# Optimization experiments

Hardware: AMD Instinct MI355X
Metric: run time of the kernel (lower is better)

The kernel has to match this reference:

```python
import jax, jax.numpy as jnp
import numpy as np

B, S, F, H = 16, 2048, 1024, 16
D = F // H
EPS = 1e-5


def setup_inputs() -> dict:
    key = jax.random.key(0)
    ks = jax.random.split(key, 10)
    scale = 1.0 / np.sqrt(F)
    return {
        "x": jax.random.normal(ks[0], (B, S, F), jnp.float32),
        "Wq": jax.random.normal(ks[1], (F, F), jnp.float32) * scale,
        "bq": jnp.zeros((F,), jnp.float32),
        "Wk": jax.random.normal(ks[2], (F, F), jnp.float32) * scale,
        "bk": jnp.zeros((F,), jnp.float32),
        "Wv": jax.random.normal(ks[3], (F, F), jnp.float32) * scale,
        "bv": jnp.zeros((F,), jnp.float32),
        "Wo": jax.random.normal(ks[4], (F, F), jnp.float32) * scale,
        "bo": jnp.zeros((F,), jnp.float32),
        "gamma": jnp.ones((F,), jnp.float32),
        "beta": jnp.zeros((F,), jnp.float32),
    }


def reference(x, Wq, bq, Wk, bk, Wv, bv, Wo, bo, gamma, beta):
    # x: (B, S, F). Dropout is identity in eval mode.
    b, s, f = x.shape
    q = (x @ Wq + bq).reshape(b, s, H, D)
    k = (x @ Wk + bk).reshape(b, s, H, D)
    v = (x @ Wv + bv).reshape(b, s, H, D)
    # Faithful to source: the einsum (applied to permuted tensors) contracts
    # across HEADS at each sequence position -> scores (B, S, H, H).
    energy = jnp.einsum('bshd,bsgd->bshg', q, k) / (D ** 0.5)
    attn = jax.nn.softmax(energy, axis=-1)  # softmax over key-head axis
    out = jnp.einsum('bshg,bsgd->bshd', attn, v).reshape(b, s, f)
    out = out @ Wo + bo
    # LayerNorm over last dim (eps=1e-5, affine)
    mu = jnp.mean(out, axis=-1, keepdims=True)
    var = jnp.mean((out - mu) ** 2, axis=-1, keepdims=True)
    return (out - mu) * jax.lax.rsqrt(var + EPS) * gamma + beta
```

## Files before the change

### kernel.cpp

```cpp
#include <hip/hip_runtime.h>
#include <hip/hip_bf16.h>
#include <stdint.h>

#define MM   32768
#define FFD  1024
#define NQKV 3072

typedef __bf16 bf16x8 __attribute__((ext_vector_type(8)));
typedef float  f32x4  __attribute__((ext_vector_type(4)));

__device__ __forceinline__ unsigned short f2bf_bits(float f){
  __hip_bfloat16 h = __float2bfloat16(f);
  unsigned short u;
  __builtin_memcpy(&u, &h, 2);
  return u;
}

__device__ __forceinline__ void gld16(const void* g, void* l){
  const unsigned int* gu = (const unsigned int*)g;
  unsigned int* lu = (unsigned int*)l;
  __builtin_amdgcn_global_load_lds(
      (const __attribute__((address_space(1))) unsigned int*)gu,
      (__attribute__((address_space(3))) unsigned int*)lu,
      16, 0, 0);
}

__global__ __launch_bounds__(256) void k_convert_bf16(const float* __restrict__ in,
                                                      unsigned short* __restrict__ out,
                                                      int n4){
  int i = blockIdx.x * 256 + threadIdx.x;
  if (i >= n4) return;
  float4 v = ((const float4*)in)[i];
  ushort4 r;
  r.x = f2bf_bits(v.x); r.y = f2bf_bits(v.y);
  r.z = f2bf_bits(v.z); r.w = f2bf_bits(v.w);
  ((ushort4*)out)[i] = r;
}

__global__ __launch_bounds__(256) void k_transpose_bf16(const float* __restrict__ in,
                                                        unsigned short* __restrict__ out,
                                                        int rows, int cols){
  __shared__ float tile[32][33];
  int bc = blockIdx.x * 32, br = blockIdx.y * 32;
  int tx = threadIdx.x, ty = threadIdx.y;
  #pragma unroll
  for (int j = 0; j < 32; j += 8)
    tile[ty + j][tx] = in[(size_t)(br + ty + j) * cols + bc + tx];
  __syncthreads();
  #pragma unroll
  for (int j = 0; j < 32; j += 8)
    out[(size_t)(bc + ty + j) * rows + br + tx] = f2bf_bits(tile[tx][ty + j]);
}

template <bool BF16OUT>
__global__ __launch_bounds__(256) void k_gemm_bt(
    const unsigned short* __restrict__ A,
    const unsigned short* __restrict__ Bt,
    const float* __restrict__ b0, const float* __restrict__ b1, const float* __restrict__ b2,
    void* __restrict__ Cout, int M, int N, int K)
{
  __shared__ unsigned short As[128 * 64];
  __shared__ unsigned short Bs[128 * 64];

  const int tid  = threadIdx.x;
  const int lane = tid & 63;
  const int wave = tid >> 6;
  const int wr = wave >> 1, wc = wave & 1;
  const int quad = lane >> 4, lrow = lane & 15;

  const long rowBase = (long)blockIdx.y * 128;
  const long colBase = (long)blockIdx.x * 128;

  f32x4 acc[4][4];
  #pragma unroll
  for (int i = 0; i < 4; i++)
    #pragma unroll
    for (int j = 0; j < 4; j++)
      acc[i][j] = (f32x4){0.f, 0.f, 0.f, 0.f};

  const unsigned short* ga = A  + (rowBase + (tid >> 2)) * (long)K + (tid & 3) * 8;
  const unsigned short* gb = Bt + (colBase + (tid >> 2)) * (long)K + (tid & 3) * 8;
  unsigned short* la = As + tid * 8;
  unsigned short* lb = Bs + tid * 8;
  const long rstep = 64L * K;

  const int nk = K >> 6;
  for (int kt = 0; kt < nk; kt++){
    __syncthreads();
    gld16(ga,               la);
    gld16(ga + rstep,       la + 2048);
    gld16(ga + 32,          la + 4096);
    gld16(ga + 32 + rstep,  la + 6144);
    gld16(gb,               lb);
    gld16(gb + rstep,       lb + 2048);
    gld16(gb + 32,          lb + 4096);
    gld16(gb + 32 + rstep,  lb + 6144);
    __syncthreads();

    #pragma unroll
    for (int kk = 0; kk < 2; kk++){
      const unsigned short* Ah = As + kk * 4096;
      const unsigned short* Bh = Bs + kk * 4096;
      bf16x8 af[4], bfr[4];
      #pragma unroll
      for (int i = 0; i < 4; i++)
        af[i]  = *(const bf16x8*)(Ah + (wr * 64 + i * 16 + lrow) * 32 + quad * 8);
      #pragma unroll
      for (int j = 0; j < 4; j++)
        bfr[j] = *(const bf16x8*)(Bh + (wc * 64 + j * 16 + lrow) * 32 + quad * 8);

      #pragma unroll
      for (int i = 0; i < 4; i++)
        #pragma unroll
        for (int j = 0; j < 4; j++)
          acc[i][j] = __builtin_amdgcn_mfma_f32_16x16x32_bf16(af[i], bfr[j], acc[i][j], 0, 0, 0);
    }

    ga += 64; gb += 64;
  }

  #pragma unroll
  for (int j = 0; j < 4; j++){
    long col = colBase + wc * 64 + j * 16 + lrow;
    const float* bp = (col < 1024) ? b0 : ((col < 2048) ? b1 : b2);
    float bias = bp[col & 1023];
    #pragma unroll
    for (int i = 0; i < 4; i++){
      long row0 = rowBase + wr * 64 + i * 16 + quad * 4;
      #pragma unroll
      for (int r = 0; r < 4; r++){
        float v = acc[i][j][r] + bias;
        if constexpr (BF16OUT)
          ((unsigned short*)Cout)[(row0 + r) * (long)N + col] = f2bf_bits(v);
        else
          ((float*)Cout)[(row0 + r) * (long)N + col] = v;
      }
    }
  }
}

__global__ __launch_bounds__(256) void k_attention(const unsigned short* __restrict__ qkv,
                                                   unsigned short* __restrict__ aout){
  constexpr int QOFF = 0;
  constexpr int KOFF = 1152;
  constexpr int VOFF = 2304;
  constexpr int POFF = 4864;
  constexpr int PER  = 5504;
  __shared__ unsigned short smem[4 * PER];

  const int lane = threadIdx.x & 63;
  const int wave = threadIdx.x >> 6;
  const int pos  = blockIdx.x * 4 + wave;
  const int quad = lane >> 4, lidx = lane & 15;

  unsigned short* base = smem + wave * PER;
  unsigned short* Qb = base + QOFF;
  unsigned short* Kb = base + KOFF;
  unsigned short* Vt = base + VOFF;
  unsigned short* Pb = base + POFF;

  {
    uint4 z = {0u, 0u, 0u, 0u};
    *(uint4*)(Vt + lane * 40 + 16) = z;
    *(uint4*)(Vt + lane * 40 + 24) = z;
    *(uint2*)(Pb + (lane >> 2) * 40 + 16 + (lane & 3) * 4) = make_uint2(0u, 0u);
  }

  const unsigned short* src = qkv + (size_t)pos * 3072;
  #pragma unroll
  for (int i = 0; i < 6; i++){
    int c = i * 64 + lane;
    uint4 u = *(const uint4*)(src + c * 8);
    if (i < 4){
      unsigned short* mb = (c < 128) ? Qb : Kb;
      int cc = c & 127;
      *(uint4*)(mb + (cc >> 3) * 72 + (cc & 7) * 8) = u;
    } else {
      int cv = c - 256;
      int g = cv >> 3, d0 = (cv & 7) * 8;
      const unsigned short* us = (const unsigned short*)&u;
      #pragma unroll
      for (int t = 0; t < 8; t++) Vt[(d0 + t) * 40 + g] = us[t];
    }
  }
  __syncthreads();

  f32x4 s = (f32x4){0.f, 0.f, 0.f, 0.f};
  #pragma unroll
  for (int kk = 0; kk < 2; kk++){
    bf16x8 a = *(const bf16x8*)(Qb + lidx * 72 + kk * 32 + quad * 8);
    bf16x8 b = *(const bf16x8*)(Kb + lidx * 72 + kk * 32 + quad * 8);
    s = __builtin_amdgcn_mfma_f32_16x16x32_bf16(a, b, s, 0, 0, 0);
  }

  #pragma unroll
  for (int r = 0; r < 4; r++){
    float v = s[r] * 0.125f;
    float m = v;
    m = fmaxf(m, __shfl_xor(m, 1));
    m = fmaxf(m, __shfl_xor(m, 2));
    m = fmaxf(m, __shfl_xor(m, 4));
    m = fmaxf(m, __shfl_xor(m, 8));
    float e = __expf(v - m);
    float sum = e;
    sum += __shfl_xor(sum, 1);
    sum += __shfl_xor(sum, 2);
    sum += __shfl_xor(sum, 4);
    sum += __shfl_xor(sum, 8);
    float p = e / sum;
    Pb[(quad * 4 + r) * 40 + lidx] = f2bf_bits(p);
  }
  __syncthreads();

  f32x4 o[4];
  #pragma unroll
  for (int n4 = 0; n4 < 4; n4++){
    bf16x8 a = *(const bf16x8*)(Pb + lidx * 40 + quad * 8);
    bf16x8 b = *(const bf16x8*)(Vt + (n4 * 16 + lidx) * 40 + quad * 8);
    o[n4] = __builtin_amdgcn_mfma_f32_16x16x32_bf16(a, b, (f32x4){0.f,0.f,0.f,0.f}, 0, 0, 0);
  }

  #pragma unroll
  for (int n4 = 0; n4 < 4; n4++)
    #pragma unroll
    for (int r = 0; r < 4; r++)
      Qb[(quad * 4 + r) * 72 + n4 * 16 + lidx] = f2bf_bits(o[n4][r]);
  __syncthreads();

  unsigned short* dst = aout + (size_t)pos * 1024;
  #pragma unroll
  for (int t = 0; t < 2; t++){
    int j = lane * 2 + t;
    int h = j >> 3, dc = j & 7;
    uint4 u = *(const uint4*)(Qb + h * 72 + dc * 8);
    *(uint4*)(dst + j * 8) = u;
  }
}

__global__ __launch_bounds__(256) void k_ln(float* __restrict__ out,
                                            const float* __restrict__ gamma,
                                            const float* __restrict__ beta){
  __shared__ float red[8];
  int tid = threadIdx.x;
  float4* rowp = (float4*)(out + (size_t)blockIdx.x * 1024);
  float4 v = rowp[tid];
  float s  = v.x + v.y + v.z + v.w;
  float ss = v.x * v.x + v.y * v.y + v.z * v.z + v.w * v.w;
  #pragma unroll
  for (int off = 32; off > 0; off >>= 1){
    s  += __shfl_down(s, off);
    ss += __shfl_down(ss, off);
  }
  if ((tid & 63) == 0){ red[tid >> 6] = s; red[4 + (tid >> 6)] = ss; }
  __syncthreads();
  float S  = red[0] + red[1] + red[2] + red[3];
  float SS = red[4] + red[5] + red[6] + red[7];
  float mean = S * (1.0f / 1024.0f);
  float var  = SS * (1.0f / 1024.0f) - mean * mean;
  float rstd = rsqrtf(var + 1e-5f);
  float4 g = ((const float4*)gamma)[tid];
  float4 b = ((const float4*)beta)[tid];
  v.x = (v.x - mean) * rstd * g.x + b.x;
  v.y = (v.y - mean) * rstd * g.y + b.y;
  v.z = (v.z - mean) * rstd * g.z + b.z;
  v.w = (v.w - mean) * rstd * g.w + b.w;
  rowp[tid] = v;
}

extern "C" void kernel_launch(void* const* d_in, const int* in_sizes, int n_in,
                              void* d_out, int out_size, void* d_ws, size_t ws_size,
                              hipStream_t stream){
  const float* x     = (const float*)d_in[0];
  const float* Wq    = (const float*)d_in[1];
  const float* bq    = (const float*)d_in[2];
  const float* Wk    = (const float*)d_in[3];
  const float* bk    = (const float*)d_in[4];
  const float* Wv    = (const float*)d_in[5];
  const float* bv    = (const float*)d_in[6];
  const float* Wo    = (const float*)d_in[7];
  const float* bo    = (const float*)d_in[8];
  const float* gamma = (const float*)d_in[9];
  const float* beta  = (const float*)d_in[10];
  float* out = (float*)d_out;

  char* ws = (char*)d_ws;
  unsigned short* Wqkv_t = (unsigned short*)ws;
  unsigned short* Wo_t   = (unsigned short*)(ws + 6291456);
  unsigned short* xb     = (unsigned short*)(ws + 8388608);
  unsigned short* qkv    = (unsigned short*)(ws + 75497472);
  unsigned short* aout   = xb;

  k_convert_bf16<<<32768, 256, 0, stream>>>(x, xb, (MM * FFD) / 4);

  dim3 tb(32, 8), tg(32, 32);
  k_transpose_bf16<<<tg, tb, 0, stream>>>(Wq, Wqkv_t,                1024, 1024);
  k_transpose_bf16<<<tg, tb, 0, stream>>>(Wk, Wqkv_t + 1024 * 1024,  1024, 1024);
  k_transpose_bf16<<<tg, tb, 0, stream>>>(Wv, Wqkv_t + 2048 * 1024,  1024, 1024);
  k_transpose_bf16<<<tg, tb, 0, stream>>>(Wo, Wo_t,                  1024, 1024);

  k_gemm_bt<true><<<dim3(NQKV / 128, MM / 128), 256, 0, stream>>>(
      xb, Wqkv_t, bq, bk, bv, qkv, MM, NQKV, FFD);

  k_attention<<<MM / 4, 256, 0, stream>>>(qkv, aout);

  k_gemm_bt<false><<<dim3(FFD / 128, MM / 128), 256, 0, stream>>>(
      aout, Wo_t, bo, bo, bo, out, MM, FFD, FFD);

  k_ln<<<MM, 256, 0, stream>>>(out, gamma, beta);
}
```

Measured before the change: 704.1 us.

## Fuse output projection GEMM with LayerNorm and merge weight transposes

Replaces the second GEMM plus separate LayerNorm kernel with a kernel where each 512-thread block computes 64 complete output rows across all 1024 columns, adds bias, reduces mean/variance via shuffles and LDS, and writes normalized fp32 output directly. This removes a full fp32 round trip of the output tensor through memory and one launch. It also merges the four weight-transpose launches into one using blockIdx.z. The large 64KB B tile in LDS and single-buffered K loop reduce occupancy and latency hiding, and every block rereads all of Wo.

```diff
diff --git a/kernel.cpp b/kernel.cpp
--- a/kernel.cpp
+++ b/kernel.cpp
@@ -37,27 +37,36 @@
   ((ushort4*)out)[i] = r;
 }
 
-__global__ __launch_bounds__(256) void k_transpose_bf16(const float* __restrict__ in,
-                                                        unsigned short* __restrict__ out,
-                                                        int rows, int cols){
+__global__ __launch_bounds__(256) void k_transpose4(
+    const float* __restrict__ W0, const float* __restrict__ W1,
+    const float* __restrict__ W2, const float* __restrict__ W3,
+    unsigned short* __restrict__ D0, unsigned short* __restrict__ D1,
+    unsigned short* __restrict__ D2, unsigned short* __restrict__ D3){
   __shared__ float tile[32][33];
+  const float* in;
+  unsigned short* out;
+  switch (blockIdx.z){
+    case 0:  in = W0; out = D0; break;
+    case 1:  in = W1; out = D1; break;
+    case 2:  in = W2; out = D2; break;
+    default: in = W3; out = D3; break;
+  }
   int bc = blockIdx.x * 32, br = blockIdx.y * 32;
   int tx = threadIdx.x, ty = threadIdx.y;
   #pragma unroll
   for (int j = 0; j < 32; j += 8)
-    tile[ty + j][tx] = in[(size_t)(br + ty + j) * cols + bc + tx];
+    tile[ty + j][tx] = in[(size_t)(br + ty + j) * 1024 + bc + tx];
   __syncthreads();
   #pragma unroll
   for (int j = 0; j < 32; j += 8)
-    out[(size_t)(bc + ty + j) * rows + br + tx] = f2bf_bits(tile[tx][ty + j]);
-}
-
-template <bool BF16OUT>
+    out[(size_t)(bc + ty + j) * 1024 + br + tx] = f2bf_bits(tile[tx][ty + j]);
+}
+
 __global__ __launch_bounds__(256) void k_gemm_bt(
     const unsigned short* __restrict__ A,
     const unsigned short* __restrict__ Bt,
     const float* __restrict__ b0, const float* __restrict__ b1, const float* __restrict__ b2,
-    void* __restrict__ Cout, int M, int N, int K)
+    unsigned short* __restrict__ Cout, int M, int N, int K)
 {
   __shared__ unsigned short As[128 * 64];
   __shared__ unsigned short Bs[128 * 64];
@@ -130,13 +139,139 @@
       #pragma unroll
       for (int r = 0; r < 4; r++){
         float v = acc[i][j][r] + bias;
-        if constexpr (BF16OUT)
-          ((unsigned short*)Cout)[(row0 + r) * (long)N + col] = f2bf_bits(v);
-        else
-          ((float*)Cout)[(row0 + r) * (long)N + col] = v;
+        Cout[(row0 + r) * (long)N + col] = f2bf_bits(v);
       }
     }
   }
+}
+
+__global__ __launch_bounds__(512) void k_gemm2_ln(
+    const unsigned short* __restrict__ A,
+    const unsigned short* __restrict__ Bt,
+    const float* __restrict__ bo,
+    const float* __restrict__ gamma,
+    const float* __restrict__ beta,
+    float* __restrict__ out)
+{
+  __shared__ unsigned short Bs[1024 * 32];
+  __shared__ unsigned short As[64 * 32];
+  __shared__ float redS[64 * 8];
+  __shared__ float redQ[64 * 8];
+  __shared__ float redM[64];
+  __shared__ float redR[64];
+
+  const int tid  = threadIdx.x;
+  const int lane = tid & 63;
+  const int wave = tid >> 6;
+  const int quad = lane >> 4, lidx = lane & 15;
+  const long rowBase = (long)blockIdx.x * 64;
+  const int K = 1024;
+
+  f32x4 acc[4][8];
+  #pragma unroll
+  for (int i = 0; i < 4; i++)
+    #pragma unroll
+    for (int j = 0; j < 8; j++)
+      acc[i][j] = (f32x4){0.f, 0.f, 0.f, 0.f};
+
+  const unsigned short* gb = Bt + (tid >> 2) * (long)K + (tid & 3) * 8;
+  unsigned short* lb = Bs + tid * 8;
+  const unsigned short* ga = A + (rowBase + (tid >> 2)) * (long)K + (tid & 3) * 8;
+  unsigned short* la = As + tid * 8;
+
+  for (int kt = 0; kt < 32; kt++){
+    __syncthreads();
+    #pragma unroll
+    for (int i = 0; i < 8; i++)
+      gld16(gb + i * (128L * K), lb + i * 4096);
+    if (tid < 256) gld16(ga, la);
+    __syncthreads();
+
+    bf16x8 af[4], bfr[8];
+    #pragma unroll
+    for (int i = 0; i < 4; i++)
+      af[i] = *(const bf16x8*)(As + (i * 16 + lidx) * 32 + quad * 8);
+    #pragma unroll
+    for (int j = 0; j < 8; j++)
+      bfr[j] = *(const bf16x8*)(Bs + (wave * 128 + j * 16 + lidx) * 32 + quad * 8);
+
+    #pragma unroll
+    for (int i = 0; i < 4; i++)
+      #pragma unroll
+      for (int j = 0; j < 8; j++)
+        acc[i][j] = __builtin_amdgcn_mfma_f32_16x16x32_bf16(af[i], bfr[j], acc[i][j], 0, 0, 0);
+
+    gb += 32; ga += 32;
+  }
+
+  float bias[8], gmm[8], btt[8];
+  #pragma unroll
+  for (int j = 0; j < 8; j++){
+    int col = wave * 128 + j * 16 + lidx;
+    bias[j] = bo[col]; gmm[j] = gamma[col]; btt[j] = beta[col];
+  }
+
+  float s1[4][4], s2[4][4];
+  #pragma unroll
+  for (int i = 0; i < 4; i++)
+    #pragma unroll
+    for (int r = 0; r < 4; r++){ s1[i][r] = 0.f; s2[i][r] = 0.f; }
+
+  #pragma unroll
+  for (int i = 0; i < 4; i++)
+    #pragma unroll
+    for (int j = 0; j < 8; j++)
+      #pragma unroll
+      for (int r = 0; r < 4; r++){
+        float v = acc[i][j][r] + bias[j];
+        acc[i][j][r] = v;
+        s1[i][r] += v;
+        s2[i][r] += v * v;
+      }
+
+  #pragma unroll
+  for (int off = 1; off < 16; off <<= 1){
+    #pragma unroll
+    for (int i = 0; i < 4; i++)
+      #pragma unroll
+      for (int r = 0; r < 4; r++){
+        s1[i][r] += __shfl_xor(s1[i][r], off);
+        s2[i][r] += __shfl_xor(s2[i][r], off);
+      }
+  }
+  if (lidx == 0){
+    #pragma unroll
+    for (int i = 0; i < 4; i++)
+      #pragma unroll
+      for (int r = 0; r < 4; r++){
+        int row = i * 16 + quad * 4 + r;
+        redS[row * 8 + wave] = s1[i][r];
+        redQ[row * 8 + wave] = s2[i][r];
+      }
+  }
+  __syncthreads();
+  if (tid < 64){
+    float S = 0.f, Q = 0.f;
+    #pragma unroll
+    for (int w = 0; w < 8; w++){ S += redS[tid * 8 + w]; Q += redQ[tid * 8 + w]; }
+    float mean = S * (1.0f / 1024.0f);
+    float var  = Q * (1.0f / 1024.0f) - mean * mean;
+    redM[tid] = mean;
+    redR[tid] = rsqrtf(var + 1e-5f);
+  }
+  __syncthreads();
+
+  #pragma unroll
+  for (int i = 0; i < 4; i++)
+    #pragma unroll
+    for (int r = 0; r < 4; r++){
+      int row = i * 16 + quad * 4 + r;
+      float mean = redM[row], rstd = redR[row];
+      float* orow = out + (rowBase + row) * 1024L + wave * 128;
+      #pragma unroll
+      for (int j = 0; j < 8; j++)
+        orow[j * 16 + lidx] = (acc[i][j][r] - mean) * rstd * gmm[j] + btt[j];
+    }
 }
 
 __global__ __launch_bounds__(256) void k_attention(const unsigned short* __restrict__ qkv,
@@ -237,36 +372,6 @@
   }
 }
 
-__global__ __launch_bounds__(256) void k_ln(float* __restrict__ out,
-                                            const float* __restrict__ gamma,
-                                            const float* __restrict__ beta){
-  __shared__ float red[8];
-  int tid = threadIdx.x;
-  float4* rowp = (float4*)(out + (size_t)blockIdx.x * 1024);
-  float4 v = rowp[tid];
-  float s  = v.x + v.y + v.z + v.w;
-  float ss = v.x * v.x + v.y * v.y + v.z * v.z + v.w * v.w;
-  #pragma unroll
-  for (int off = 32; off > 0; off >>= 1){
-    s  += __shfl_down(s, off);
-    ss += __shfl_down(ss, off);
-  }
-  if ((tid & 63) == 0){ red[tid >> 6] = s; red[4 + (tid >> 6)] = ss; }
-  __syncthreads();
-  float S  = red[0] + red[1] + red[2] + red[3];
-  float SS = red[4] + red[5] + red[6] + red[7];
-  float mean = S * (1.0f / 1024.0f);
-  float var  = SS * (1.0f / 1024.0f) - mean * mean;
-  float rstd = rsqrtf(var + 1e-5f);
-  float4 g = ((const float4*)gamma)[tid];
-  float4 b = ((const float4*)beta)[tid];
-  v.x = (v.x - mean) * rstd * g.x + b.x;
-  v.y = (v.y - mean) * rstd * g.y + b.y;
-  v.z = (v.z - mean) * rstd * g.z + b.z;
-  v.w = (v.w - mean) * rstd * g.w + b.w;
-  rowp[tid] = v;
-}
-
 extern "C" void kernel_launch(void* const* d_in, const int* in_sizes, int n_in,
                               void* d_out, int out_size, void* d_ws, size_t ws_size,
                               hipStream_t stream){
@@ -292,19 +397,14 @@
 
   k_convert_bf16<<<32768, 256, 0, stream>>>(x, xb, (MM * FFD) / 4);
 
-  dim3 tb(32, 8), tg(32, 32);
-  k_transpose_bf16<<<tg, tb, 0, stream>>>(Wq, Wqkv_t,                1024, 1024);
-  k_transpose_bf16<<<tg, tb, 0, stream>>>(Wk, Wqkv_t + 1024 * 1024,  1024, 1024);
-  k_transpose_bf16<<<tg, tb, 0, stream>>>(Wv, Wqkv_t + 2048 * 1024,  1024, 1024);
-  k_transpose_bf16<<<tg, tb, 0, stream>>>(Wo, Wo_t,                  1024, 1024);
-
-  k_gemm_bt<true><<<dim3(NQKV / 128, MM / 128), 256, 0, stream>>>(
+  k_transpose4<<<dim3(32, 32, 4), dim3(32, 8), 0, stream>>>(
+      Wq, Wk, Wv, Wo,
+      Wqkv_t, Wqkv_t + 1024 * 1024, Wqkv_t + 2048 * 1024, Wo_t);
+
+  k_gemm_bt<<<dim3(NQKV / 128, MM / 128), 256, 0, stream>>>(
       xb, Wqkv_t, bq, bk, bv, qkv, MM, NQKV, FFD);
 
   k_attention<<<MM / 4, 256, 0, stream>>>(qkv, aout);
 
-  k_gemm_bt<false><<<dim3(FFD / 128, MM / 128), 256, 0, stream>>>(
-      aout, Wo_t, bo, bo, bo, out, MM, FFD, FFD);
-
-  k_ln<<<MM, 256, 0, stream>>>(out, gamma, beta);
-}
+  k_gemm2_ln<<<MM / 64, 512, 0, stream>>>(aout, Wo_t, bo, gamma, beta, out);
+}
```

Result: slower. 719.8 us (+2.2%).
